# Optimization experiments

Hardware: AMD Instinct MI355X
Metric: run time of the kernel (lower is better)

The kernel has to match this reference:

```python
import jax, jax.numpy as jnp
import numpy as np

D_MODEL = 192
D_INNER = 384          # expand * d_model
D_STATE = 64
NHEADS = 8             # d_inner / headdim
HEADDIM = 48
D_CONV = 4
CONV_DIM = D_INNER + 2 * D_STATE   # 512 (ngroups=1)
D_IN_PROJ = 2 * D_INNER + 2 * D_STATE + NHEADS  # 904
MIX = 32
EPS = 1e-5


def silu(v):
    return v * jax.nn.sigmoid(v)


def setup_inputs() -> dict:
    key = jax.random.key(0)
    ks = jax.random.split(key, 16)
    B, L, C = 4, 4096, 4
    x = jax.random.normal(ks[0], (B, L, C), jnp.float32)
    Wfc = jax.random.normal(ks[1], (C, D_MODEL), jnp.float32) * 0.3
    bfc = jnp.zeros((D_MODEL,), jnp.float32)
    W_in = jax.random.normal(ks[2], (D_MODEL, D_IN_PROJ), jnp.float32) * 0.02
    conv_w = jax.random.normal(ks[3], (D_CONV, 1, CONV_DIM), jnp.float32) * 0.2  # depthwise (W,I/g,O)
    conv_b = jnp.zeros((CONV_DIM,), jnp.float32)
    # dt_bias = inv_softplus(dt_init) with dt_init ~ U(1e-3, 0.1)
    dt_init = jax.random.uniform(ks[4], (NHEADS,), jnp.float32, 1e-3, 0.1)
    dt_bias = jnp.log(jnp.expm1(dt_init))
    A_log = jnp.log(jax.random.uniform(ks[5], (NHEADS,), jnp.float32, 1.0, 16.0))
    Dparam = jnp.ones((NHEADS,), jnp.float32)
    norm_w = jnp.ones((D_INNER,), jnp.float32)
    W_out = jax.random.normal(ks[6], (D_INNER, D_MODEL), jnp.float32) * 0.02
    W1 = jax.random.normal(ks[7], (D_MODEL, MIX), jnp.float32) * 0.05
    b1 = jnp.zeros((MIX,), jnp.float32)
    W2 = jax.random.normal(ks[8], (MIX, MIX), jnp.float32) * 0.1
    b2 = jnp.zeros((MIX,), jnp.float32)
    Wo = jax.random.normal(ks[9], (MIX, 1), jnp.float32) * 0.1
    bo = jnp.zeros((1,), jnp.float32)
    return {"x": x, "Wfc": Wfc, "bfc": bfc, "W_in": W_in, "conv_w": conv_w,
            "conv_b": conv_b, "dt_bias": dt_bias, "A_log": A_log, "Dparam": Dparam,
            "norm_w": norm_w, "W_out": W_out, "W1": W1, "b1": b1, "W2": W2,
            "b2": b2, "Wo": Wo, "bo": bo}


def _mamba2(h, W_in, conv_w, conv_b, dt_bias, A_log, Dparam, norm_w, W_out):
    B, L, _ = h.shape
    zxbcdt = h @ W_in                                    # (B,L,904)
    z = zxbcdt[..., :D_INNER]
    xBC = zxbcdt[..., D_INNER:D_INNER + CONV_DIM]
    dt = jax.nn.softplus(zxbcdt[..., -NHEADS:] + dt_bias)  # (B,L,H)
    # causal depthwise conv1d
    xBC = jnp.pad(xBC, ((0, 0), (D_CONV - 1, 0), (0, 0)))
    xBC = jax.lax.conv_general_dilated(
        xBC, conv_w, window_strides=(1,), padding="VALID",
        dimension_numbers=("NWC", "WIO", "NWC"), feature_group_count=CONV_DIM)
    xBC = silu(xBC + conv_b)                             # (B,L,512)
    xs = xBC[..., :D_INNER].reshape(B, L, NHEADS, HEADDIM)
    Bm = xBC[..., D_INNER:D_INNER + D_STATE]             # (B,L,N)
    Cm = xBC[..., D_INNER + D_STATE:]                    # (B,L,N)
    A = -jnp.exp(A_log)                                  # (H,)
    dA = jnp.exp(dt * A)                                 # (B,L,H)

    def step(hstate, inp):
        dA_t, dt_t, B_t, x_t, C_t = inp                  # (B,H),(B,H),(B,N),(B,H,P),(B,N)
        dBx_t = jnp.einsum("bh,bn,bhp->bhpn", dt_t, B_t, x_t)
        hstate = dA_t[:, :, None, None] * hstate + dBx_t  # (B,H,P,N)
        y_t = jnp.einsum("bhpn,bn->bhp", hstate, C_t)
        return hstate, y_t

    h0 = jnp.zeros((B, NHEADS, HEADDIM, D_STATE), h.dtype)
    xs_t = jnp.swapaxes(xs, 0, 1)
    _, ys = jax.lax.scan(step, h0, (jnp.swapaxes(dA, 0, 1), jnp.swapaxes(dt, 0, 1),
                                    jnp.swapaxes(Bm, 0, 1), xs_t, jnp.swapaxes(Cm, 0, 1)))
    y = jnp.swapaxes(ys, 0, 1) + Dparam[None, None, :, None] * xs  # (B,L,H,P)
    y = y.reshape(B, L, D_INNER)
    # gated RMSNorm: rmsnorm(y * silu(z)) * weight
    y = y * silu(z)
    y = y * jax.lax.rsqrt(jnp.mean(y * y, axis=-1, keepdims=True) + EPS) * norm_w
    return y @ W_out                                     # (B,L,d_model)


def reference(x, Wfc, bfc, W_in, conv_w, conv_b, dt_bias, A_log, Dparam,
              norm_w, W_out, W1, b1, W2, b2, Wo, bo):
    h = x @ Wfc + bfc                                    # input_fc
    h = _mamba2(h, W_in, conv_w, conv_b, dt_bias, A_log, Dparam, norm_w, W_out)
    m = jax.nn.relu(h @ W1 + b1)
    m = jax.nn.relu(m @ W2 + b2)                         # dropout = identity (eval)
    m = jnp.mean(m, axis=1)                              # pool over time
    angle = (m @ Wo + bo)[:, 0]
    return angle
```

## Files before the change

kernel.cpp:

```cpp
#include <hip/hip_runtime.h>
#include <math.h>


#define BDIM 4
#define LDIM 4096
#define BL (BDIM*LDIM)
#define QC 64
#define NC (LDIM/QC)
#define BH (BDIM*NH)
#define NH 8

#define OFF_W    0u
#define OFF_Z    3145728u
#define OFF_T    9437184u
#define OFF_XS   17825792u
#define OFF_BM   24117248u
#define OFF_CM   25165824u
#define OFF_DT   26214400u
#define OFF_LAC  26345472u
#define OFF_SP   26476544u
#define OFF_Y    32768000u
#define OFF_MACC 39059456u

typedef unsigned short ushort_t;
typedef __attribute__((ext_vector_type(8))) short bf16x8;
typedef __attribute__((ext_vector_type(4))) float f32x4;

__device__ __forceinline__ float sigmoidf_(float x){ return 1.0f/(1.0f+__expf(-x)); }
__device__ __forceinline__ ushort_t f2bf(float x){
  unsigned int u = __float_as_uint(x);
  u += 0x7fffu + ((u>>16)&1u);
  return (ushort_t)(u>>16);
}
__device__ __forceinline__ float bf2f(ushort_t h){
  return __uint_as_float(((unsigned int)h)<<16);
}

__global__ void k_prep(const float* __restrict__ Wfc, const float* __restrict__ bfc,
                       const float* __restrict__ W_in, const float* __restrict__ W_out,
                       const float* __restrict__ W1, const float* __restrict__ norm_w,
                       float* __restrict__ Weff, float* __restrict__ beff,
                       float* __restrict__ Weff2, float* __restrict__ macc){
  int blk = blockIdx.x, tid = threadIdx.x;
  if (blk < 4){
    int n = blk*256 + tid;
    if (n >= 904) return;
    float a0=0.f,a1=0.f,a2=0.f,a3=0.f,ab=0.f;
    for (int d=0; d<192; d++){
      float w = W_in[(size_t)d*904 + n];
      a0 = fmaf(Wfc[d], w, a0);
      a1 = fmaf(Wfc[192+d], w, a1);
      a2 = fmaf(Wfc[384+d], w, a2);
      a3 = fmaf(Wfc[576+d], w, a3);
      ab = fmaf(bfc[d], w, ab);
    }
    Weff[n] = a0; Weff[904+n] = a1; Weff[1808+n] = a2; Weff[2712+n] = a3;
    beff[n] = ab;
  } else {
    if (blk == 4 && tid < 128) macc[tid] = 0.f;
    int g = (blk-4)*256 + tid;
    int i = g>>5, j = g&31;
    float a = 0.f;
    for (int d=0; d<192; d++) a = fmaf(W_out[(size_t)i*192+d], W1[d*32+j], a);
    Weff2[g] = a * norm_w[i];
  }
}

__global__ __launch_bounds__(256) void k_ipc(
    const float* __restrict__ x, const float* __restrict__ Weff,
    const float* __restrict__ beff, const float* __restrict__ conv_w,
    const float* __restrict__ conv_b, const float* __restrict__ dt_bias,
    ushort_t* __restrict__ xs_h, ushort_t* __restrict__ xs_l,
    ushort_t* __restrict__ Bm_h, ushort_t* __restrict__ Bm_l,
    ushort_t* __restrict__ Cm_h, ushort_t* __restrict__ Cm_l,
    float* __restrict__ dtb){
  __shared__ float sx[7][4];
  int pb = blockIdx.x, tid = threadIdx.x;
  int bl0 = pb*4;
  int l0 = bl0 & 4095, b = bl0 >> 12;
  if (tid < 28){
    int row = tid>>2, r = tid&3;
    int ll = l0-3+row;
    sx[row][r] = (ll>=0) ? x[(size_t)(b*4096+ll)*4 + r] : 0.f;
  }
  __syncthreads();
  if (tid < 32){
    int t = tid>>3, hh = tid&7;
    float raw = beff[896+hh];
    #pragma unroll
    for (int r=0;r<4;r++) raw = fmaf(sx[3+t][r], Weff[r*904+896+hh], raw);
    float xx = raw + dt_bias[hh];
    float dtv = (xx > 20.f) ? xx : log1pf(__expf(xx));
    dtb[(size_t)(b*8+hh)*4096 + l0 + t] = dtv;
  }
  #pragma unroll
  for (int half=0; half<2; half++){
    int c = tid + half*256;
    float w0 = Weff[384+c];
    float w1 = Weff[904+384+c];
    float w2 = Weff[1808+384+c];
    float w3 = Weff[2712+384+c];
    float bb = beff[384+c];
    float cw0 = conv_w[c], cw1 = conv_w[512+c], cw2 = conv_w[1024+c], cw3 = conv_w[1536+c];
    float cb = conv_b[c];
    float pre[7];
    #pragma unroll
    for (int q=0;q<7;q++){
      int ll = l0-3+q;
      float xv = bb;
      xv = fmaf(sx[q][0], w0, xv);
      xv = fmaf(sx[q][1], w1, xv);
      xv = fmaf(sx[q][2], w2, xv);
      xv = fmaf(sx[q][3], w3, xv);
      pre[q] = (ll >= 0) ? xv : 0.f;
    }
    float av[4];
    #pragma unroll
    for (int t=0;t<4;t++){
      float a = cb;
      a = fmaf(cw0,pre[t+0],a); a = fmaf(cw1,pre[t+1],a);
      a = fmaf(cw2,pre[t+2],a); a = fmaf(cw3,pre[t+3],a);
      av[t] = a * sigmoidf_(a);
    }
    if (c < 384){
      int hh = c / 48, p = c - hh*48;
      size_t idx = (size_t)((b*8+hh)*4096 + l0)*48 + p;
      #pragma unroll
      for (int t=0;t<4;t++){
        ushort_t h = f2bf(av[t]);
        xs_h[idx + t*48] = h;
        xs_l[idx + t*48] = f2bf(av[t] - bf2f(h));
      }
    } else if (c < 448){
      size_t idx = (size_t)bl0*64 + (c-384);
      #pragma unroll
      for (int t=0;t<4;t++){
        ushort_t h = f2bf(av[t]);
        Bm_h[idx + t*64] = h;
        Bm_l[idx + t*64] = f2bf(av[t] - bf2f(h));
      }
    } else {
      size_t idx = (size_t)bl0*64 + (c-448);
      #pragma unroll
      for (int t=0;t<4;t++){
        ushort_t h = f2bf(av[t]);
        Cm_h[idx + t*64] = h;
        Cm_l[idx + t*64] = f2bf(av[t] - bf2f(h));
      }
    }
  }
}

__global__ __launch_bounds__(256, 3) void k_phase1(
    const float* __restrict__ dtbuf,
    const ushort_t* __restrict__ Bm_h, const ushort_t* __restrict__ Bm_l,
    const ushort_t* __restrict__ xs_h, const ushort_t* __restrict__ xs_l,
    const float* __restrict__ A_log,
    ushort_t* __restrict__ T, float* __restrict__ lac){
  __shared__ __align__(16) ushort_t sBh[64*72], sBl[64*72];
  __shared__ __align__(16) ushort_t sXh[48*72], sXl[48*72];
  __shared__ float sdt[64], sla[64], sw[64];
  int tid = threadIdx.x, blk = blockIdx.x;
  int bh = blk >> 6, k = blk & 63;
  int b = bh >> 3, hh = bh & 7;
  int t0 = k*64;
  int w = tid>>6, lane = tid&63, l15 = lane&15, quad = lane>>4;

  if (tid < 64) sdt[tid] = dtbuf[(size_t)bh*4096 + t0 + tid];
  __syncthreads();
  if (tid == 0){
    float eA = __expf(A_log[hh]);
    float cum = 0.f;
    for (int i=0;i<64;i++){ cum -= sdt[i]*eA; sla[i] = cum; }
  }
  __syncthreads();
  if (tid < 64){
    sw[tid] = __expf(sla[63]-sla[tid])*sdt[tid];
    lac[(size_t)blk*64 + tid] = sla[tid];
  }
  __syncthreads();
  {
    int s2 = (tid&31)*2, ng = (tid>>5)*8;
    size_t base0 = (size_t)(b*4096+t0+s2)*64 + ng;
    ushort_t h0a[8], l0a[8], h1a[8], l1a[8];
    *(uint4*)h0a = *(const uint4*)(Bm_h + base0);
    *(uint4*)l0a = *(const uint4*)(Bm_l + base0);
    *(uint4*)h1a = *(const uint4*)(Bm_h + base0 + 64);
    *(uint4*)l1a = *(const uint4*)(Bm_l + base0 + 64);
    float w0 = sw[s2], w1 = sw[s2+1];
    #pragma unroll
    for (int c=0;c<8;c++){
      float f0 = (bf2f(h0a[c]) + bf2f(l0a[c])) * w0;
      float f1 = (bf2f(h1a[c]) + bf2f(l1a[c])) * w1;
      ushort_t h0 = f2bf(f0), h1 = f2bf(f1);
      ushort_t lo0 = f2bf(f0-bf2f(h0)), lo1 = f2bf(f1-bf2f(h1));
      int o = (ng+c)*72 + s2;
      *(unsigned int*)&sBh[o] = (unsigned int)h0 | ((unsigned int)h1<<16);
      *(unsigned int*)&sBl[o] = (unsigned int)lo0 | ((unsigned int)lo1<<16);
    }
  }
  {
    int s2 = (tid>>3)*2, p0 = (tid&7)*6;
    const ushort_t* xh0 = xs_h + (size_t)(bh*4096+t0+s2)*48 + p0;
    const ushort_t* xl0 = xs_l + (size_t)(bh*4096+t0+s2)*48 + p0;
    #pragma unroll
    for (int c=0;c<6;c++){
      unsigned int hv = (unsigned int)xh0[c] | ((unsigned int)xh0[48+c]<<16);
      unsigned int lv = (unsigned int)xl0[c] | ((unsigned int)xl0[48+c]<<16);
      int o = (p0+c)*72 + s2;
      *(unsigned int*)&sXh[o] = hv;
      *(unsigned int*)&sXl[o] = lv;
    }
  }
  __syncthreads();
  f32x4 acc[3];
  #pragma unroll
  for (int t=0;t<3;t++) acc[t] = (f32x4)(0.f);
  #pragma unroll
  for (int ks=0;ks<2;ks++){
    int bo = (w*16+l15)*72 + ks*32 + quad*8;
    bf16x8 bbh = *(bf16x8*)&sBh[bo];
    bf16x8 bbl = *(bf16x8*)&sBl[bo];
    #pragma unroll
    for (int pt=0;pt<3;pt++){
      int xo = (pt*16+l15)*72 + ks*32 + quad*8;
      bf16x8 xah = *(bf16x8*)&sXh[xo];
      bf16x8 xal = *(bf16x8*)&sXl[xo];
      acc[pt] = __builtin_amdgcn_mfma_f32_16x16x32_bf16(xah, bbh, acc[pt], 0,0,0);
      acc[pt] = __builtin_amdgcn_mfma_f32_16x16x32_bf16(xah, bbl, acc[pt], 0,0,0);
      acc[pt] = __builtin_amdgcn_mfma_f32_16x16x32_bf16(xal, bbh, acc[pt], 0,0,0);
    }
  }
  {
    ushort_t* dst = T + (size_t)blk*3072;
    #pragma unroll
    for (int pt=0;pt<3;pt++)
      #pragma unroll
      for (int r=0;r<4;r++)
        dst[(pt*16+quad*4+r)*64 + w*16 + l15] = f2bf(acc[pt][r]);
  }
}

__global__ __launch_bounds__(256) void k_phase2p(
    const ushort_t* __restrict__ T, const float* __restrict__ lac,
    ushort_t* __restrict__ Sp){
  __shared__ __align__(16) float sT[64*64];
  __shared__ __align__(16) float sW[64][68];
  __shared__ float sc[64];
  int tid = threadIdx.x;
  int bh = blockIdx.x, es = blockIdx.y;
  #pragma unroll
  for (int r=0;r<2;r++){
    int idx = tid + r*256;
    int row = idx>>3, g8 = (idx&7)*8;
    ushort_t tv[8];
    *(uint4*)tv = *(const uint4*)(T + (size_t)(bh*64+row)*3072 + es*64 + g8);
    #pragma unroll
    for (int c=0;c<8;c++) sT[row*64 + g8 + c] = bf2f(tv[c]);
  }
  if (tid < 64) sc[tid] = __expf(lac[(size_t)(bh*64+tid)*64 + 63]);
  __syncthreads();
  if (tid < 64){
    int k = tid;
    float w = 1.f;
    for (int j=63; j>=0; --j){
      bool a = (j < k);
      sW[j][k] = a ? w : 0.f;
      if (a) w *= sc[j];
    }
  }
  __syncthreads();
  int k0 = (tid>>4)*4, e0 = (tid&15)*4;
  float acc[4][4];
  #pragma unroll
  for (int i=0;i<4;i++)
    #pragma unroll
    for (int j=0;j<4;j++) acc[i][j]=0.f;
  int jmax = k0+2; if (jmax > 62) jmax = 62;
  for (int j=0; j<=jmax; ++j){
    float wv[4], tv[4];
    *(float4*)wv = *(float4*)&sW[j][k0];
    *(float4*)tv = *(float4*)&sT[j*64 + e0];
    #pragma unroll
    for (int i=0;i<4;i++)
      #pragma unroll
      for (int e=0;e<4;e++) acc[i][e] = fmaf(wv[i], tv[e], acc[i][e]);
  }
  #pragma unroll
  for (int i=0;i<4;i++){
    ushort4 h4;
    ushort_t* hp = (ushort_t*)&h4;
    #pragma unroll
    for (int e=0;e<4;e++) hp[e] = f2bf(acc[i][e]);
    *(ushort4*)(Sp + (size_t)(bh*64+k0+i)*3072 + es*64 + e0) = h4;
  }
}

__global__ __launch_bounds__(256, 3) void k_phase3(
    const float* __restrict__ dtbuf, const float* __restrict__ lac,
    const ushort_t* __restrict__ Bm_h, const ushort_t* __restrict__ Bm_l,
    const ushort_t* __restrict__ Cm_h, const ushort_t* __restrict__ Cm_l,
    const ushort_t* __restrict__ xs_h, const ushort_t* __restrict__ xs_l,
    const ushort_t* __restrict__ Sp, const float* __restrict__ Dparam,
    ushort_t* __restrict__ y16){
  __shared__ __align__(16) ushort_t sCh[64*72], sCl[64*72];
  __shared__ __align__(16) ushort_t sBh[64*72], sBl[64*72];
  __shared__ __align__(16) ushort_t sXh[48*72], sXl[48*72];
  __shared__ float sla[64], sdt[64];
  int tid = threadIdx.x, blk = blockIdx.x;
  int bh = blk>>6, k = blk&63, b = bh>>3, hh = bh&7, t0 = k*64;
  int w = tid>>6, lane = tid&63, l15 = lane&15, quad = lane>>4;

  if (tid < 64){
    sdt[tid] = dtbuf[(size_t)bh*4096 + t0 + tid];
    sla[tid] = lac[(size_t)blk*64 + tid];
  }
  {
    int row = tid>>2, ng = (tid&3)*16;
    size_t gb = (size_t)(b*4096+t0+row)*64 + ng;
    int o = row*72 + ng;
    *(uint4*)&sCh[o]   = *(const uint4*)(Cm_h + gb);
    *(uint4*)&sCh[o+8] = *(const uint4*)(Cm_h + gb + 8);
    *(uint4*)&sCl[o]   = *(const uint4*)(Cm_l + gb);
    *(uint4*)&sCl[o+8] = *(const uint4*)(Cm_l + gb + 8);
    *(uint4*)&sBh[o]   = *(const uint4*)(Bm_h + gb);
    *(uint4*)&sBh[o+8] = *(const uint4*)(Bm_h + gb + 8);
    *(uint4*)&sBl[o]   = *(const uint4*)(Bm_l + gb);
    *(uint4*)&sBl[o+8] = *(const uint4*)(Bm_l + gb + 8);
  }
  {
    int s2 = (tid>>3)*2, p0 = (tid&7)*6;
    const ushort_t* xh0 = xs_h + (size_t)(bh*4096+t0+s2)*48 + p0;
    const ushort_t* xl0 = xs_l + (size_t)(bh*4096+t0+s2)*48 + p0;
    #pragma unroll
    for (int c=0;c<6;c++){
      unsigned int hv = (unsigned int)xh0[c] | ((unsigned int)xh0[48+c]<<16);
      unsigned int lv = (unsigned int)xl0[c] | ((unsigned int)xl0[48+c]<<16);
      int o = (p0+c)*72 + s2;
      *(unsigned int*)&sXh[o] = hv;
      *(unsigned int*)&sXl[o] = lv;
    }
  }
  __syncthreads();

  f32x4 gacc[4];
  #pragma unroll
  for (int t=0;t<4;t++) gacc[t] = (f32x4)(0.f);
  {
    bf16x8 cah[2], cal[2];
    #pragma unroll
    for (int ks=0;ks<2;ks++){
      int ao = (w*16+l15)*72 + ks*32 + quad*8;
      cah[ks] = *(bf16x8*)&sCh[ao];
      cal[ks] = *(bf16x8*)&sCl[ao];
    }
    for (int bs=0; bs<=w; ++bs){
      #pragma unroll
      for (int ks=0;ks<2;ks++){
        int bo = (bs*16+l15)*72 + ks*32 + quad*8;
        bf16x8 bhf = *(bf16x8*)&sBh[bo];
        bf16x8 blf = *(bf16x8*)&sBl[bo];
        gacc[bs] = __builtin_amdgcn_mfma_f32_16x16x32_bf16(cah[ks], bhf, gacc[bs], 0,0,0);
        gacc[bs] = __builtin_amdgcn_mfma_f32_16x16x32_bf16(cah[ks], blf, gacc[bs], 0,0,0);
        gacc[bs] = __builtin_amdgcn_mfma_f32_16x16x32_bf16(cal[ks], bhf, gacc[bs], 0,0,0);
      }
    }
  }
  __syncthreads();

  for (int bs=0; bs<=w; ++bs){
    #pragma unroll
    for (int r=0;r<4;r++){
      int i = w*16 + quad*4 + r;
      int s = bs*16 + l15;
      float v = 0.f;
      if (s <= i) v = gacc[bs][r] * __expf(sla[i]-sla[s]) * sdt[s];
      sBh[i*72+s] = f2bf(v);
    }
  }
  if (w==0){
    #pragma unroll
    for (int r=0;r<4;r++) sBh[(quad*4+r)*72 + 16+l15] = 0;
  }
  if (w==2){
    #pragma unroll
    for (int r=0;r<4;r++) sBh[(32+quad*4+r)*72 + 48+l15] = 0;
  }
  __syncthreads();

  bf16x8 pah[3][2];
  {
    const ushort_t* sph = Sp + (size_t)blk*3072;
    #pragma unroll
    for (int pt=0;pt<3;pt++)
      #pragma unroll
      for (int ks=0;ks<2;ks++)
        pah[pt][ks] = *(const bf16x8*)(sph + (size_t)(pt*16+l15)*64 + ks*32 + quad*8);
  }

  f32x4 accI[3], accA[3];
  #pragma unroll
  for (int t=0;t<3;t++){ accI[t] = (f32x4)(0.f); accA[t] = (f32x4)(0.f); }
  int nks = (w>=2) ? 2 : 1;
  for (int ks=0; ks<nks; ++ks){
    int go = (w*16+l15)*72 + ks*32 + quad*8;
    bf16x8 gbh = *(bf16x8*)&sBh[go];
    #pragma unroll
    for (int pt=0;pt<3;pt++){
      int xo = (pt*16+l15)*72 + ks*32 + quad*8;
      bf16x8 xah = *(bf16x8*)&sXh[xo];
      bf16x8 xal = *(bf16x8*)&sXl[xo];
      accI[pt] = __builtin_amdgcn_mfma_f32_16x16x32_bf16(xah, gbh, accI[pt], 0,0,0);
      accI[pt] = __builtin_amdgcn_mfma_f32_16x16x32_bf16(xal, gbh, accI[pt], 0,0,0);
    }
  }
  #pragma unroll
  for (int ks=0; ks<2; ++ks){
    int co = (w*16+l15)*72 + ks*32 + quad*8;
    bf16x8 cbh = *(bf16x8*)&sCh[co];
    bf16x8 cbl = *(bf16x8*)&sCl[co];
    #pragma unroll
    for (int pt=0;pt<3;pt++){
      accA[pt] = __builtin_amdgcn_mfma_f32_16x16x32_bf16(pah[pt][ks], cbh, accA[pt], 0,0,0);
      accA[pt] = __builtin_amdgcn_mfma_f32_16x16x32_bf16(pah[pt][ks], cbl, accA[pt], 0,0,0);
    }
  }
  {
    int i = w*16 + l15;
    float eli = __expf(sla[i]);
    float Dh = Dparam[hh];
    ushort_t* ybase = y16 + (size_t)(b*4096+t0+i)*384 + hh*48;
    #pragma unroll
    for (int pt=0;pt<3;pt++)
      #pragma unroll
      for (int r=0;r<4;r++){
        int p = pt*16 + quad*4 + r;
        float xf = bf2f(sXh[p*72 + i]) + bf2f(sXl[p*72 + i]);
        ybase[p] = f2bf(accI[pt][r] + eli*accA[pt][r] + Dh*xf);
      }
  }
}

__global__ __launch_bounds__(256) void k_gate(
    const float* __restrict__ x, const float* __restrict__ Weff,
    const float* __restrict__ beff,
    const ushort_t* __restrict__ y16, ushort_t* __restrict__ yn16){
  int tid = threadIdx.x;
  int w = tid>>6, lane = tid&63;
  int e0 = lane*6;
  float W0[6],W1v[6],W2v[6],W3v[6],bv[6];
  #pragma unroll
  for (int c=0;c<6;c++){
    int e = e0+c;
    W0[c]=Weff[e]; W1v[c]=Weff[904+e]; W2v[c]=Weff[1808+e]; W3v[c]=Weff[2712+e];
    bv[c]=beff[e];
  }
  #pragma unroll
  for (int t=0;t<4;t++){
    int bl = blockIdx.x*16 + w*4 + t;
    float4 xv = *(const float4*)(x + (size_t)bl*4);
    float g[6]; float ss = 0.f;
    #pragma unroll
    for (int c=0;c<6;c++){
      float zv = bv[c];
      zv = fmaf(xv.x, W0[c], zv);
      zv = fmaf(xv.y, W1v[c], zv);
      zv = fmaf(xv.z, W2v[c], zv);
      zv = fmaf(xv.w, W3v[c], zv);
      float yv = bf2f(y16[(size_t)bl*384 + e0 + c]);
      float gg = yv * (zv * sigmoidf_(zv));
      g[c] = gg; ss += gg*gg;
    }
    #pragma unroll
    for (int off=32; off>0; off>>=1) ss += __shfl_xor(ss, off);
    float rms = rsqrtf(ss*(1.f/384.f) + 1e-5f);
    #pragma unroll
    for (int c=0;c<6;c++)
      yn16[(size_t)bl*384 + e0 + c] = f2bf(g[c]*rms);
  }
}

__global__ __launch_bounds__(256) void k_mlp2(
    const ushort_t* __restrict__ yn16, const float* __restrict__ Weff2,
    const float* __restrict__ b1, const float* __restrict__ W2,
    const float* __restrict__ b2, float* __restrict__ macc){
  __shared__ __align__(16) float sW[384][32];
  __shared__ __align__(16) float sm1[64][33];
  __shared__ __align__(16) float sW2[32][32];
  __shared__ __align__(16) float sm2[64][33];
  int tid = threadIdx.x;
  int tok0 = blockIdx.x*64;
  int b = tok0 >> 12;
  #pragma unroll
  for (int r=0;r<12;r++){
    int idx = tid + r*256;
    int row = idx>>3, c4 = (idx&7)*4;
    *(float4*)&sW[row][c4] = *(const float4*)(Weff2 + (size_t)idx*4);
  }
  {
    int row = tid>>3, c4 = (tid&7)*4;
    *(float4*)&sW2[row][c4] = *(const float4*)(W2 + row*32 + c4);
  }
  __syncthreads();
  {
    int tk = tid>>3, j0 = (tid&7)*4;
    float a0[4], a1[4];
    #pragma unroll
    for (int j=0;j<4;j++){ a0[j] = b1[j0+j]; a1[j] = a0[j]; }
    const ushort_t* y0 = yn16 + (size_t)(tok0+tk)*384;
    const ushort_t* y1 = yn16 + (size_t)(tok0+tk+32)*384;
    for (int k8=0;k8<48;k8++){
      ushort_t ua[8], ub[8];
      *(uint4*)ua = *(const uint4*)(y0 + k8*8);
      *(uint4*)ub = *(const uint4*)(y1 + k8*8);
      #pragma unroll
      for (int c=0;c<8;c++){
        float va = bf2f(ua[c]), vb = bf2f(ub[c]);
        float w[4]; *(float4*)w = *(float4*)&sW[k8*8+c][j0];
        #pragma unroll
        for (int j=0;j<4;j++){ a0[j] = fmaf(va, w[j], a0[j]); a1[j] = fmaf(vb, w[j], a1[j]); }
      }
    }
    #pragma unroll
    for (int j=0;j<4;j++){
      sm1[tk][j0+j]    = fmaxf(a0[j], 0.f);
      sm1[tk+32][j0+j] = fmaxf(a1[j], 0.f);
    }
  }
  __syncthreads();
  {
    int tk = tid>>3, j0 = (tid&7)*4;
    float a0[4], a1[4];
    #pragma unroll
    for (int j=0;j<4;j++){ a0[j] = b2[j0+j]; a1[j] = a0[j]; }
    #pragma unroll
    for (int kk=0;kk<32;kk++){
      float va = sm1[tk][kk];
      float vb = sm1[tk+32][kk];
      float w[4]; *(float4*)w = *(float4*)&sW2[kk][j0];
      #pragma unroll
      for (int j=0;j<4;j++){ a0[j] = fmaf(va, w[j], a0[j]); a1[j] = fmaf(vb, w[j], a1[j]); }
    }
    #pragma unroll
    for (int j=0;j<4;j++){
      sm2[tk][j0+j]    = fmaxf(a0[j], 0.f);
      sm2[tk+32][j0+j] = fmaxf(a1[j], 0.f);
    }
  }
  __syncthreads();
  if (tid < 32){
    float t = 0.f;
    #pragma unroll
    for (int tok=0;tok<64;tok++) t += sm2[tok][tid];
    atomicAdd(&macc[b*32 + tid], t);
  }
}

__global__ void k_final(const float* __restrict__ macc, const float* __restrict__ Wo,
                        const float* __restrict__ bo, float* __restrict__ out){
  int tid = threadIdx.x;
  if (tid < 4){
    float acc = bo[0];
    #pragma unroll
    for (int j=0;j<32;j++) acc = fmaf(macc[tid*32+j]*(1.f/4096.f), Wo[j], acc);
    out[tid] = acc;
  }
}

extern "C" void kernel_launch(void* const* d_in, const int* in_sizes, int n_in,
                              void* d_out, int out_size, void* d_ws, size_t ws_size,
                              hipStream_t stream){
  const float* x      = (const float*)d_in[0];
  const float* Wfc    = (const float*)d_in[1];
  const float* bfc    = (const float*)d_in[2];
  const float* W_in   = (const float*)d_in[3];
  const float* conv_w = (const float*)d_in[4];
  const float* conv_b = (const float*)d_in[5];
  const float* dt_bias= (const float*)d_in[6];
  const float* A_log  = (const float*)d_in[7];
  const float* Dparam = (const float*)d_in[8];
  const float* norm_w = (const float*)d_in[9];
  const float* W_out  = (const float*)d_in[10];
  const float* W1     = (const float*)d_in[11];
  const float* b1     = (const float*)d_in[12];
  const float* W2     = (const float*)d_in[13];
  const float* b2     = (const float*)d_in[14];
  const float* Wo     = (const float*)d_in[15];
  const float* bo     = (const float*)d_in[16];
  float* ws  = (float*)d_ws;
  float* out = (float*)d_out;

  float* Weff  = ws + OFF_W;
  float* beff  = ws + OFF_W + 4096;
  float* Weff2 = ws + OFF_W + 8192;
  ushort_t* yn16 = (ushort_t*)(ws + OFF_Z);
  ushort_t* Tb   = (ushort_t*)(ws + OFF_T);
  ushort_t* xs_h = (ushort_t*)(ws + OFF_XS);
  ushort_t* xs_l = xs_h + 6291456u;
  ushort_t* Bm_h = (ushort_t*)(ws + OFF_BM);
  ushort_t* Bm_l = Bm_h + 1048576u;
  ushort_t* Cm_h = (ushort_t*)(ws + OFF_CM);
  ushort_t* Cm_l = Cm_h + 1048576u;
  float* dtb   = ws + OFF_DT;
  float* lacb  = ws + OFF_LAC;
  ushort_t* Spb  = (ushort_t*)(ws + OFF_SP);
  ushort_t* y16 = (ushort_t*)(ws + OFF_Y);
  float* macc  = ws + OFF_MACC;

  k_prep<<<dim3(52), dim3(256), 0, stream>>>(Wfc, bfc, W_in, W_out, W1, norm_w,
                                             Weff, beff, Weff2, macc);
  k_ipc<<<dim3(BL/4), dim3(256), 0, stream>>>(x, Weff, beff, conv_w, conv_b,
                                              dt_bias, xs_h, xs_l, Bm_h, Bm_l,
                                              Cm_h, Cm_l, dtb);
  k_phase1<<<dim3(BH*NC), dim3(256), 0, stream>>>(dtb, Bm_h, Bm_l, xs_h, xs_l,
                                                  A_log, Tb, lacb);
  k_phase2p<<<dim3(BH,48), dim3(256), 0, stream>>>(Tb, lacb, Spb);
  k_phase3<<<dim3(BH*NC), dim3(256), 0, stream>>>(dtb, lacb, Bm_h, Bm_l,
                                                  Cm_h, Cm_l, xs_h, xs_l,
                                                  Spb, Dparam, y16);
  k_gate<<<dim3(BL/16), dim3(256), 0, stream>>>(x, Weff, beff, y16, yn16);
  k_mlp2<<<dim3(BL/64), dim3(256), 0, stream>>>(yn16, Weff2, b1, W2, b2, macc);
  k_final<<<dim3(1), dim3(64), 0, stream>>>(macc, Wo, bo, out);
}
```

Measured before the change: 189.5 us.

## Fuse SiLU gating and RMS sum into scan output, apply norm in MLP

```diff
diff --git a/kernel.cpp b/kernel.cpp
--- a/kernel.cpp
+++ b/kernel.cpp
@@ -40,7 +40,8 @@
                        const float* __restrict__ W_in, const float* __restrict__ W_out,
                        const float* __restrict__ W1, const float* __restrict__ norm_w,
                        float* __restrict__ Weff, float* __restrict__ beff,
-                       float* __restrict__ Weff2, float* __restrict__ macc){
+                       float* __restrict__ Weff2, float* __restrict__ macc,
+                       float* __restrict__ ssum){
   int blk = blockIdx.x, tid = threadIdx.x;
   if (blk < 4){
     int n = blk*256 + tid;
@@ -56,13 +57,16 @@
     }
     Weff[n] = a0; Weff[904+n] = a1; Weff[1808+n] = a2; Weff[2712+n] = a3;
     beff[n] = ab;
-  } else {
+  } else if (blk < 52){
     if (blk == 4 && tid < 128) macc[tid] = 0.f;
     int g = (blk-4)*256 + tid;
     int i = g>>5, j = g&31;
     float a = 0.f;
     for (int d=0; d<192; d++) a = fmaf(W_out[(size_t)i*192+d], W1[d*32+j], a);
     Weff2[g] = a * norm_w[i];
+  } else {
+    int idx = (blk-52)*256 + tid;
+    ssum[idx] = 0.f;
   }
 }
 
@@ -302,7 +306,9 @@
     const ushort_t* __restrict__ Cm_h, const ushort_t* __restrict__ Cm_l,
     const ushort_t* __restrict__ xs_h, const ushort_t* __restrict__ xs_l,
     const ushort_t* __restrict__ Sp, const float* __restrict__ Dparam,
-    ushort_t* __restrict__ y16){
+    const float* __restrict__ xg, const float* __restrict__ Weff,
+    const float* __restrict__ beff,
+    ushort_t* __restrict__ g16, float* __restrict__ ssum){
   __shared__ __align__(16) ushort_t sCh[64*72], sCl[64*72];
   __shared__ __align__(16) ushort_t sBh[64*72], sBl[64*72];
   __shared__ __align__(16) ushort_t sXh[48*72], sXl[48*72];
@@ -427,63 +433,40 @@
   }
   {
     int i = w*16 + l15;
+    int tok = b*4096 + t0 + i;
     float eli = __expf(sla[i]);
     float Dh = Dparam[hh];
-    ushort_t* ybase = y16 + (size_t)(b*4096+t0+i)*384 + hh*48;
+    float4 xv = *(const float4*)(xg + (size_t)tok*4);
+    ushort_t* gbase = g16 + (size_t)tok*384 + hh*48;
+    float ssq = 0.f;
     #pragma unroll
     for (int pt=0;pt<3;pt++)
       #pragma unroll
       for (int r=0;r<4;r++){
         int p = pt*16 + quad*4 + r;
         float xf = bf2f(sXh[p*72 + i]) + bf2f(sXl[p*72 + i]);
-        ybase[p] = f2bf(accI[pt][r] + eli*accA[pt][r] + Dh*xf);
+        float yv = accI[pt][r] + eli*accA[pt][r] + Dh*xf;
+        int e = hh*48 + p;
+        float zv = beff[e];
+        zv = fmaf(xv.x, Weff[e], zv);
+        zv = fmaf(xv.y, Weff[904+e], zv);
+        zv = fmaf(xv.z, Weff[1808+e], zv);
+        zv = fmaf(xv.w, Weff[2712+e], zv);
+        float gg = yv * (zv * sigmoidf_(zv));
+        gbase[p] = f2bf(gg);
+        ssq += gg*gg;
       }
-  }
-}
-
-__global__ __launch_bounds__(256) void k_gate(
-    const float* __restrict__ x, const float* __restrict__ Weff,
-    const float* __restrict__ beff,
-    const ushort_t* __restrict__ y16, ushort_t* __restrict__ yn16){
-  int tid = threadIdx.x;
-  int w = tid>>6, lane = tid&63;
-  int e0 = lane*6;
-  float W0[6],W1v[6],W2v[6],W3v[6],bv[6];
-  #pragma unroll
-  for (int c=0;c<6;c++){
-    int e = e0+c;
-    W0[c]=Weff[e]; W1v[c]=Weff[904+e]; W2v[c]=Weff[1808+e]; W3v[c]=Weff[2712+e];
-    bv[c]=beff[e];
-  }
-  #pragma unroll
-  for (int t=0;t<4;t++){
-    int bl = blockIdx.x*16 + w*4 + t;
-    float4 xv = *(const float4*)(x + (size_t)bl*4);
-    float g[6]; float ss = 0.f;
-    #pragma unroll
-    for (int c=0;c<6;c++){
-      float zv = bv[c];
-      zv = fmaf(xv.x, W0[c], zv);
-      zv = fmaf(xv.y, W1v[c], zv);
-      zv = fmaf(xv.z, W2v[c], zv);
-      zv = fmaf(xv.w, W3v[c], zv);
-      float yv = bf2f(y16[(size_t)bl*384 + e0 + c]);
-      float gg = yv * (zv * sigmoidf_(zv));
-      g[c] = gg; ss += gg*gg;
-    }
-    #pragma unroll
-    for (int off=32; off>0; off>>=1) ss += __shfl_xor(ss, off);
-    float rms = rsqrtf(ss*(1.f/384.f) + 1e-5f);
-    #pragma unroll
-    for (int c=0;c<6;c++)
-      yn16[(size_t)bl*384 + e0 + c] = f2bf(g[c]*rms);
+    ssq += __shfl_xor(ssq, 16);
+    ssq += __shfl_xor(ssq, 32);
+    if (quad == 0) atomicAdd(&ssum[tok], ssq);
   }
 }
 
 __global__ __launch_bounds__(256) void k_mlp2(
-    const ushort_t* __restrict__ yn16, const float* __restrict__ Weff2,
-    const float* __restrict__ b1, const float* __restrict__ W2,
-    const float* __restrict__ b2, float* __restrict__ macc){
+    const ushort_t* __restrict__ g16, const float* __restrict__ ssum,
+    const float* __restrict__ Weff2, const float* __restrict__ b1,
+    const float* __restrict__ W2, const float* __restrict__ b2,
+    float* __restrict__ macc){
   __shared__ __align__(16) float sW[384][32];
   __shared__ __align__(16) float sm1[64][33];
   __shared__ __align__(16) float sW2[32][32];
@@ -504,18 +487,20 @@
   __syncthreads();
   {
     int tk = tid>>3, j0 = (tid&7)*4;
+    float rms0 = rsqrtf(ssum[tok0+tk]*(1.f/384.f) + 1e-5f);
+    float rms1 = rsqrtf(ssum[tok0+tk+32]*(1.f/384.f) + 1e-5f);
     float a0[4], a1[4];
     #pragma unroll
     for (int j=0;j<4;j++){ a0[j] = b1[j0+j]; a1[j] = a0[j]; }
-    const ushort_t* y0 = yn16 + (size_t)(tok0+tk)*384;
-    const ushort_t* y1 = yn16 + (size_t)(tok0+tk+32)*384;
+    const ushort_t* y0 = g16 + (size_t)(tok0+tk)*384;
+    const ushort_t* y1 = g16 + (size_t)(tok0+tk+32)*384;
     for (int k8=0;k8<48;k8++){
       ushort_t ua[8], ub[8];
       *(uint4*)ua = *(const uint4*)(y0 + k8*8);
       *(uint4*)ub = *(const uint4*)(y1 + k8*8);
       #pragma unroll
       for (int c=0;c<8;c++){
-        float va = bf2f(ua[c]), vb = bf2f(ub[c]);
+        float va = bf2f(ua[c])*rms0, vb = bf2f(ub[c])*rms1;
         float w[4]; *(float4*)w = *(float4*)&sW[k8*8+c][j0];
         #pragma unroll
         for (int j=0;j<4;j++){ a0[j] = fmaf(va, w[j], a0[j]); a1[j] = fmaf(vb, w[j], a1[j]); }
@@ -593,7 +578,7 @@
   float* Weff  = ws + OFF_W;
   float* beff  = ws + OFF_W + 4096;
   float* Weff2 = ws + OFF_W + 8192;
-  ushort_t* yn16 = (ushort_t*)(ws + OFF_Z);
+  float* ssum  = ws + OFF_Z;
   ushort_t* Tb   = (ushort_t*)(ws + OFF_T);
   ushort_t* xs_h = (ushort_t*)(ws + OFF_XS);
   ushort_t* xs_l = xs_h + 6291456u;
@@ -604,11 +589,11 @@
   float* dtb   = ws + OFF_DT;
   float* lacb  = ws + OFF_LAC;
   ushort_t* Spb  = (ushort_t*)(ws + OFF_SP);
-  ushort_t* y16 = (ushort_t*)(ws + OFF_Y);
+  ushort_t* g16 = (ushort_t*)(ws + OFF_Y);
   float* macc  = ws + OFF_MACC;
 
-  k_prep<<<dim3(52), dim3(256), 0, stream>>>(Wfc, bfc, W_in, W_out, W1, norm_w,
-                                             Weff, beff, Weff2, macc);
+  k_prep<<<dim3(116), dim3(256), 0, stream>>>(Wfc, bfc, W_in, W_out, W1, norm_w,
+                                              Weff, beff, Weff2, macc, ssum);
   k_ipc<<<dim3(BL/4), dim3(256), 0, stream>>>(x, Weff, beff, conv_w, conv_b,
                                               dt_bias, xs_h, xs_l, Bm_h, Bm_l,
                                               Cm_h, Cm_l, dtb);
@@ -617,8 +602,8 @@
   k_phase2p<<<dim3(BH,48), dim3(256), 0, stream>>>(Tb, lacb, Spb);
   k_phase3<<<dim3(BH*NC), dim3(256), 0, stream>>>(dtb, lacb, Bm_h, Bm_l,
                                                   Cm_h, Cm_l, xs_h, xs_l,
-                                                  Spb, Dparam, y16);
-  k_gate<<<dim3(BL/16), dim3(256), 0, stream>>>(x, Weff, beff, y16, yn16);
-  k_mlp2<<<dim3(BL/64), dim3(256), 0, stream>>>(yn16, Weff2, b1, W2, b2, macc);
+                                                  Spb, Dparam, x, Weff, beff,
+                                                  g16, ssum);
+  k_mlp2<<<dim3(BL/64), dim3(256), 0, stream>>>(g16, ssum, Weff2, b1, W2, b2, macc);
   k_final<<<dim3(1), dim3(64), 0, stream>>>(macc, Wo, bo, out);
 }
```

Result: no change. 186.1 us (-1.8%).
